# Performance work log

Hardware: AMD Instinct MI355X
Metric: run time of the kernel (lower is better)

Reference implementation:

```python
import jax, jax.numpy as jnp
import numpy as np

B, H, W, NF = 2, 80, 80, 128  # batch, height, width, n_filter
CIN = 2 * NF                  # input channels (final conv outputs 2*NF and adds to x)


def _conv(x, w):
    # 3x3, stride 1, SAME, no bias; NHWC / HWIO
    return jax.lax.conv_general_dilated(
        x, w, window_strides=(1, 1), padding='SAME',
        dimension_numbers=('NHWC', 'HWIO', 'NHWC'))


def setup_inputs() -> dict:
    key = jax.random.key(0)
    ks = jax.random.split(key, 5)
    def glorot(k, shape):
        fan_in = shape[0] * shape[1] * shape[2]
        fan_out = shape[0] * shape[1] * shape[3]
        lim = np.sqrt(6.0 / (fan_in + fan_out)).astype(np.float32)
        return jax.random.uniform(k, shape, jnp.float32, -lim, lim)
    return {
        'x': jax.random.normal(ks[0], (B, H, W, CIN), jnp.float32),
        'w_theta': glorot(ks[1], (3, 3, CIN, NF)),
        'w_phi':   glorot(ks[2], (3, 3, CIN, NF)),
        'w_g':     glorot(ks[3], (3, 3, CIN, NF)),
        'w_conv':  glorot(ks[4], (3, 3, NF, CIN)),
    }


def reference(x, w_theta, w_phi, w_g, w_conv):
    b, h, w, cin = x.shape
    c = w_theta.shape[-1]  # n_filter
    n = h * w
    theta = _conv(x, w_theta).reshape(b, n, c)        # (B, N, C)
    # NOTE: Keras Reshape((n_filter,-1)) is a row-major reshape, NOT a transpose
    phi = _conv(x, w_phi).reshape(b, c, n)            # (B, C, N)
    attn = jax.nn.softmax(jnp.einsum('bnc,bcm->bnm', theta, phi), axis=-1)  # (B, N, N)
    g = _conv(x, w_g).reshape(b, n, c)                # (B, N, C)
    out = jnp.einsum('bnm,bmc->bnc', attn, g).reshape(b, h, w, c)
    out = _conv(out, w_conv)                          # (B, H, W, 2C)
    return x + out
```

## Files before the change

### kernel.cpp

```cpp
#include <hip/hip_runtime.h>
#include <hip/hip_bf16.h>

#define HH_ 80
#define WW_ 80
#define CIN_ 256
#define NF_ 128
#define NPIX_ 6400
#define NTOK_ 12800
#define NELEM_ (NTOK_ * NF_)
#define NXEL_  (NTOK_ * CIN_)
#define KW_    2304
#define KWC_   1152
#define WEL_   294912

#define KVS_    8
#define KVB_    32
#define MCHUNK_ 800
#define NIT_    25

__device__ float g_theta[NELEM_];
__device__ float g_phi  [NELEM_];
__device__ float g_gv   [NELEM_];
__device__ unsigned short g_aob[NELEM_];
__device__ unsigned short g_th_hi[NELEM_], g_th_lo[NELEM_];
__device__ unsigned short g_phT_hi[NELEM_], g_phT_lo[NELEM_];
__device__ unsigned short g_gT[NELEM_];
__device__ float g_po [KVS_ * NELEM_];
__device__ float g_pml[KVS_ * NTOK_ * 2];
__device__ unsigned short g_xh[NXEL_], g_xl[NXEL_];
__device__ unsigned short g_wtTh[WEL_], g_wtTl[WEL_];
__device__ unsigned short g_wpTh[WEL_], g_wpTl[WEL_];
__device__ unsigned short g_wgT[WEL_];
__device__ unsigned short g_wcT[WEL_];

__device__ __forceinline__ float b2f(unsigned short u) {
    union { unsigned int i; float f; } v; v.i = ((unsigned int)u) << 16; return v.f;
}
__device__ __forceinline__ unsigned short f2b(float f) {
    union { float f; unsigned int i; } v; v.f = f;
    unsigned int i = v.i;
    i += 0x7fffu + ((i >> 16) & 1u);
    return (unsigned short)(i >> 16);
}

typedef __attribute__((ext_vector_type(8))) short bf16x8;
typedef __attribute__((ext_vector_type(4))) float f32x4;

__device__ __forceinline__ f32x4 mfma16(bf16x8 a, bf16x8 b, f32x4 c) {
    return __builtin_amdgcn_mfma_f32_16x16x32_bf16(a, b, c, 0, 0, 0);
}

__global__ __launch_bounds__(256) void prep_x(const float* __restrict__ x)
{
    const int i = (blockIdx.x * 256 + threadIdx.x) * 4;
    if (i >= NXEL_) return;
    const float4 v = *(const float4*)(x + i);
    ushort4 hi, lo;
    hi.x = f2b(v.x); lo.x = f2b(v.x - b2f(hi.x));
    hi.y = f2b(v.y); lo.y = f2b(v.y - b2f(hi.y));
    hi.z = f2b(v.z); lo.z = f2b(v.z - b2f(hi.z));
    hi.w = f2b(v.w); lo.w = f2b(v.w - b2f(hi.w));
    *(ushort4*)(g_xh + i) = hi;
    *(ushort4*)(g_xl + i) = lo;
}

__global__ __launch_bounds__(256) void prep_w(
    const float* __restrict__ wt, const float* __restrict__ wp,
    const float* __restrict__ wg, const float* __restrict__ wc)
{
    const int i = blockIdx.x * 256 + threadIdx.x;
    if (i >= WEL_) return;
    {
        const int t  = i / (256 * 128);
        const int r  = i % (256 * 128);
        const int ci = r >> 7;
        const int f  = r & 127;
        const size_t d = (size_t)(t * 8 + (ci >> 5)) * 4096
                       + (size_t)f * 32 + (ci & 31);
        const float tv = wt[i];
        const unsigned short th = f2b(tv);
        g_wtTh[d] = th; g_wtTl[d] = f2b(tv - b2f(th));
        const float pv = wp[i];
        const unsigned short ph = f2b(pv);
        g_wpTh[d] = ph; g_wpTl[d] = f2b(pv - b2f(ph));
        g_wgT[d] = f2b(wg[i]);
    }
    {
        const int t  = i / (128 * 256);
        const int r  = i % (128 * 256);
        const int ci = r >> 8;
        const int f  = r & 255;
        g_wcT[(size_t)f * KWC_ + t * 128 + ci] = f2b(wc[i]);
    }
}

__global__ __launch_bounds__(512) void conv3_mfma()
{
    __shared__ __align__(16) unsigned short w_lds[5][128][40];
    __shared__ __align__(16) unsigned short x_lds[64][2][40];

    const int tid  = threadIdx.x;
    const int wv   = tid >> 6;
    const int lane = tid & 63;
    const int quad = lane >> 4;
    const int ll   = lane & 15;
    const int wp   = wv >> 2;
    const int wf   = wv & 3;
    const int P0   = blockIdx.x * 64;
    const int fb   = wf * 32;

    const int sxp = tid >> 3;
    const int sxh = (tid >> 2) & 1;
    const int sxc = (tid & 3) * 8;
    const int swf = tid >> 2;
    const int swc = (tid & 3) * 8;

    const int sp  = P0 + sxp;
    const int spb = sp / NPIX_;
    const int spl = sp % NPIX_;
    const int sph = spl / WW_;
    const int spw = spl % WW_;

    const bf16x8 ZV = {0,0,0,0,0,0,0,0};
    bf16x8 rx, rw0, rw1, rw2, rw3, rw4;

#define C3_STAGE_LOAD(s)                                                      \
    {                                                                         \
        const int t_ = (s) >> 3, kc_ = (s) & 7;                               \
        const int hh_ = sph + t_ / 3 - 1, ww_ = spw + t_ % 3 - 1;             \
        if (hh_ >= 0 && hh_ < HH_ && ww_ >= 0 && ww_ < WW_) {                 \
            const size_t src_ = ((size_t)spb * NPIX_ + hh_ * WW_ + ww_) * CIN_\
                                + kc_ * 32 + sxc;                             \
            rx = sxh ? *(const bf16x8*)(g_xl + src_)                          \
                     : *(const bf16x8*)(g_xh + src_);                         \
        } else rx = ZV;                                                       \
        const size_t ws_ = (size_t)(s) * 4096 + (size_t)swf * 32 + swc;       \
        rw0 = *(const bf16x8*)(g_wtTh + ws_);                                 \
        rw1 = *(const bf16x8*)(g_wtTl + ws_);                                 \
        rw2 = *(const bf16x8*)(g_wpTh + ws_);                                 \
        rw3 = *(const bf16x8*)(g_wpTl + ws_);                                 \
        rw4 = *(const bf16x8*)(g_wgT  + ws_);                                 \
    }

#define C3_STAGE_WRITE()                                                      \
    {                                                                         \
        *(bf16x8*)(&x_lds[sxp][sxh][sxc]) = rx;                               \
        *(bf16x8*)(&w_lds[0][swf][swc]) = rw0;                                \
        *(bf16x8*)(&w_lds[1][swf][swc]) = rw1;                                \
        *(bf16x8*)(&w_lds[2][swf][swc]) = rw2;                                \
        *(bf16x8*)(&w_lds[3][swf][swc]) = rw3;                                \
        *(bf16x8*)(&w_lds[4][swf][swc]) = rw4;                                \
    }

    f32x4 aT[2][2], aP[2][2], aG[2][2];
    #pragma unroll
    for (int pt = 0; pt < 2; ++pt)
        #pragma unroll
        for (int ft = 0; ft < 2; ++ft) {
            aT[pt][ft] = (f32x4){0.f,0.f,0.f,0.f};
            aP[pt][ft] = (f32x4){0.f,0.f,0.f,0.f};
            aG[pt][ft] = (f32x4){0.f,0.f,0.f,0.f};
        }

    C3_STAGE_LOAD(0);
    C3_STAGE_WRITE();
    __syncthreads();

    for (int s = 0; s < 72; ++s) {
        const bool pf = (s + 1 < 72);
        if (pf) C3_STAGE_LOAD(s + 1);

        bf16x8 xa[2][2];
        #pragma unroll
        for (int pt = 0; pt < 2; ++pt) {
            const int px = wp * 32 + pt * 16 + ll;
            xa[pt][0] = *(const bf16x8*)(&x_lds[px][0][quad * 8]);
            xa[pt][1] = *(const bf16x8*)(&x_lds[px][1][quad * 8]);
        }
        #pragma unroll
        for (int ft = 0; ft < 2; ++ft) {
            const int f = fb + ft * 16 + ll;
            const bf16x8 tH = *(const bf16x8*)(&w_lds[0][f][quad * 8]);
            const bf16x8 tL = *(const bf16x8*)(&w_lds[1][f][quad * 8]);
            const bf16x8 pH = *(const bf16x8*)(&w_lds[2][f][quad * 8]);
            const bf16x8 pL = *(const bf16x8*)(&w_lds[3][f][quad * 8]);
            const bf16x8 gB = *(const bf16x8*)(&w_lds[4][f][quad * 8]);
            #pragma unroll
            for (int pt = 0; pt < 2; ++pt) {
                aT[pt][ft] = mfma16(xa[pt][0], tH, aT[pt][ft]);
                aT[pt][ft] = mfma16(xa[pt][0], tL, aT[pt][ft]);
                aT[pt][ft] = mfma16(xa[pt][1], tH, aT[pt][ft]);
                aP[pt][ft] = mfma16(xa[pt][0], pH, aP[pt][ft]);
                aP[pt][ft] = mfma16(xa[pt][0], pL, aP[pt][ft]);
                aP[pt][ft] = mfma16(xa[pt][1], pH, aP[pt][ft]);
                aG[pt][ft] = mfma16(xa[pt][0], gB, aG[pt][ft]);
            }
        }

        __syncthreads();
        if (pf) C3_STAGE_WRITE();
        __syncthreads();
    }

    #pragma unroll
    for (int pt = 0; pt < 2; ++pt)
        #pragma unroll
        for (int ft = 0; ft < 2; ++ft) {
            const int f = fb + ft * 16 + ll;
            #pragma unroll
            for (int r = 0; r < 4; ++r) {
                const size_t n = P0 + wp * 32 + pt * 16 + quad * 4 + r;
                g_theta[n * NF_ + f] = aT[pt][ft][r];
                g_phi  [n * NF_ + f] = aP[pt][ft][r];
                g_gv   [n * NF_ + f] = aG[pt][ft][r];
            }
        }
#undef C3_STAGE_LOAD
#undef C3_STAGE_WRITE
}

__global__ __launch_bounds__(256) void prep_pack()
{
    const int i = blockIdx.x * 256 + threadIdx.x;
    if (i >= NELEM_) return;
    const int n  = i >> 7;
    const int c  = i & 127;
    const int b  = n / NPIX_;
    const int nl = n % NPIX_;

    const float tv = g_theta[i];
    const unsigned short th = f2b(tv);
    g_th_hi[i] = th;
    g_th_lo[i] = f2b(tv - b2f(th));

    const float pv = g_phi[i];
    const int j  = nl * 128 + c;
    const int cp = j / NPIX_;
    const int mp = j % NPIX_;
    const unsigned short phh = f2b(pv);
    const size_t o = (size_t)b * (NPIX_ * NF_) + (size_t)mp * 128 + cp;
    g_phT_hi[o] = phh;
    g_phT_lo[o] = f2b(pv - b2f(phh));

    g_gT[(size_t)b * (NPIX_ * NF_) + (size_t)c * NPIX_ + nl] = f2b(g_gv[i]);
}

__global__ __launch_bounds__(256) void attn_mfma()
{
    __shared__ __align__(16) unsigned short kh_lds[KVB_][136];
    __shared__ __align__(16) unsigned short kl_lds[KVB_][136];
    __shared__ __align__(16) unsigned short v_lds[NF_][40];
    __shared__ __align__(16) short p_lds[4][16 * 40];

    const int tid  = threadIdx.x;
    const int w    = tid >> 6;
    const int lane = tid & 63;
    const int quad = lane >> 4;
    const int ll   = lane & 15;

    const int cid = blockIdx.x & 15;
    const int qw  = blockIdx.x >> 4;
    const int b   = cid >> 3;
    const int kvs = cid & 7;
    const int R0  = b * NPIX_ + qw * 64;
    const int m_start = kvs * MCHUNK_;

    const unsigned short* phH = g_phT_hi + (size_t)b * (NPIX_ * NF_);
    const unsigned short* phL = g_phT_lo + (size_t)b * (NPIX_ * NF_);
    const unsigned short* gT  = g_gT    + (size_t)b * (NPIX_ * NF_);

    bf16x8 aH[4], aL[4];
    #pragma unroll
    for (int kk = 0; kk < 4; ++kk) {
        const size_t off = (size_t)(R0 + w * 16 + ll) * 128 + kk * 32 + quad * 8;
        aH[kk] = *(const bf16x8*)(g_th_hi + off);
        aL[kk] = *(const bf16x8*)(g_th_lo + off);
    }

    f32x4 acc[8];
    #pragma unroll
    for (int t = 0; t < 8; ++t) acc[t] = (f32x4){0.f, 0.f, 0.f, 0.f};
    float mi = -1e30f, li = 0.f;

    const int kr0 = tid >> 4;
    const int kc0 = (tid & 15) * 8;
    const int vr0 = tid >> 2;
    const int vm0 = (tid & 3) * 8;

    bf16x8 skh0, skh1, skl0, skl1, sv0, sv1;

    {
        const int m0 = m_start;
        skh0 = *(const bf16x8*)(phH + (size_t)(m0 + kr0) * 128 + kc0);
        skh1 = *(const bf16x8*)(phH + (size_t)(m0 + kr0 + 16) * 128 + kc0);
        skl0 = *(const bf16x8*)(phL + (size_t)(m0 + kr0) * 128 + kc0);
        skl1 = *(const bf16x8*)(phL + (size_t)(m0 + kr0 + 16) * 128 + kc0);
        sv0  = *(const bf16x8*)(gT + (size_t)vr0 * NPIX_ + m0 + vm0);
        sv1  = *(const bf16x8*)(gT + (size_t)(vr0 + 64) * NPIX_ + m0 + vm0);
        *(bf16x8*)(&kh_lds[kr0][kc0])      = skh0;
        *(bf16x8*)(&kh_lds[kr0 + 16][kc0]) = skh1;
        *(bf16x8*)(&kl_lds[kr0][kc0])      = skl0;
        *(bf16x8*)(&kl_lds[kr0 + 16][kc0]) = skl1;
        *(bf16x8*)(&v_lds[vr0][vm0])       = sv0;
        *(bf16x8*)(&v_lds[vr0 + 64][vm0])  = sv1;
    }
    __syncthreads();

    short* pl = &p_lds[w][0];

    for (int it = 0; it < NIT_; ++it) {
        const bool pf = (it + 1 < NIT_);
        if (pf) {
            const int m0 = m_start + (it + 1) * KVB_;
            skh0 = *(const bf16x8*)(phH + (size_t)(m0 + kr0) * 128 + kc0);
            skh1 = *(const bf16x8*)(phH + (size_t)(m0 + kr0 + 16) * 128 + kc0);
            skl0 = *(const bf16x8*)(phL + (size_t)(m0 + kr0) * 128 + kc0);
            skl1 = *(const bf16x8*)(phL + (size_t)(m0 + kr0 + 16) * 128 + kc0);
            sv0  = *(const bf16x8*)(gT + (size_t)vr0 * NPIX_ + m0 + vm0);
            sv1  = *(const bf16x8*)(gT + (size_t)(vr0 + 64) * NPIX_ + m0 + vm0);
        }

        f32x4 s[2];
        #pragma unroll
        for (int mt = 0; mt < 2; ++mt) {
            f32x4 s0 = (f32x4){0.f,0.f,0.f,0.f};
            const int mrow = mt * 16 + ll;
            #pragma unroll
            for (int kk = 0; kk < 4; ++kk) {
                const bf16x8 bH = *(const bf16x8*)(&kh_lds[mrow][kk * 32 + quad * 8]);
                const bf16x8 bL = *(const bf16x8*)(&kl_lds[mrow][kk * 32 + quad * 8]);
                s0 = mfma16(bH, aH[kk], s0);
                s0 = mfma16(bL, aH[kk], s0);
                s0 = mfma16(bH, aL[kk], s0);
            }
            s[mt] = s0;
        }

        float cm = fmaxf(fmaxf(fmaxf(s[0][0], s[0][1]), fmaxf(s[0][2], s[0][3])),
                         fmaxf(fmaxf(s[1][0], s[1][1]), fmaxf(s[1][2], s[1][3])));
        cm = fmaxf(cm, __shfl_xor(cm, 16));
        cm = fmaxf(cm, __shfl_xor(cm, 32));
        const float nm = fmaxf(mi, cm);
        const float al = __expf(mi - nm);
        mi = nm;
        float ssum = 0.f;
        #pragma unroll
        for (int mt = 0; mt < 2; ++mt)
            #pragma unroll
            for (int r = 0; r < 4; ++r) {
                const float e = __expf(s[mt][r] - nm);
                s[mt][r] = e; ssum += e;
            }
        ssum += __shfl_xor(ssum, 16);
        ssum += __shfl_xor(ssum, 32);
        li = li * al + ssum;

        if (quad == 0)
            ((float*)(pl + (ll >> 2) * 40 + 32))[ll & 3] = al;

        #pragma unroll
        for (int mt = 0; mt < 2; ++mt)
            *(ushort4*)(pl + ll * 40 + mt * 16 + quad * 4) =
                make_ushort4(f2b(s[mt][0]), f2b(s[mt][1]),
                             f2b(s[mt][2]), f2b(s[mt][3]));

        {
            const float* alp = (const float*)(pl + quad * 40 + 32);
            #pragma unroll
            for (int r = 0; r < 4; ++r) {
                const float av = alp[r];
                #pragma unroll
                for (int t = 0; t < 8; ++t) acc[t][r] *= av;
            }
        }

        const bf16x8 pa = *(const bf16x8*)(pl + ll * 40 + quad * 8);

        #pragma unroll
        for (int ct = 0; ct < 8; ++ct) {
            const bf16x8 gb = *(const bf16x8*)(&v_lds[ct * 16 + ll][quad * 8]);
            acc[ct] = mfma16(pa, gb, acc[ct]);
        }

        __syncthreads();
        if (pf) {
            *(bf16x8*)(&kh_lds[kr0][kc0])      = skh0;
            *(bf16x8*)(&kh_lds[kr0 + 16][kc0]) = skh1;
            *(bf16x8*)(&kl_lds[kr0][kc0])      = skl0;
            *(bf16x8*)(&kl_lds[kr0 + 16][kc0]) = skl1;
            *(bf16x8*)(&v_lds[vr0][vm0])       = sv0;
            *(bf16x8*)(&v_lds[vr0 + 64][vm0])  = sv1;
        }
        __syncthreads();
    }

    const int row0 = R0 + w * 16;
    #pragma unroll
    for (int ct = 0; ct < 8; ++ct)
        #pragma unroll
        for (int r = 0; r < 4; ++r)
            g_po[((size_t)kvs * NTOK_ + row0 + quad * 4 + r) * NF_ + ct * 16 + ll]
                = acc[ct][r];
    if (quad == 0) {
        const size_t mlidx = ((size_t)kvs * NTOK_ + row0 + ll) * 2;
        g_pml[mlidx]     = mi;
        g_pml[mlidx + 1] = li;
    }
}

__global__ __launch_bounds__(256) void merge_attn()
{
    const int idx = blockIdx.x * 256 + threadIdx.x;
    const int row = idx >> 4;
    const int c0  = (idx & 15) * 8;

    float m[KVS_], l[KVS_];
    #pragma unroll
    for (int s = 0; s < KVS_; ++s) {
        const size_t mlidx = ((size_t)s * NTOK_ + row) * 2;
        m[s] = g_pml[mlidx];
        l[s] = g_pml[mlidx + 1];
    }
    float M = m[0];
    #pragma unroll
    for (int s = 1; s < KVS_; ++s) M = fmaxf(M, m[s]);
    float a[KVS_], L = 0.f;
    #pragma unroll
    for (int s = 0; s < KVS_; ++s) {
        a[s] = __expf(m[s] - M);
        L += a[s] * l[s];
    }
    const float inv = 1.f / L;

    float o[8];
    #pragma unroll
    for (int j = 0; j < 8; ++j) o[j] = 0.f;
    #pragma unroll
    for (int s = 0; s < KVS_; ++s) {
        const float* p = g_po + ((size_t)s * NTOK_ + row) * NF_ + c0;
        const float4 p0 = *(const float4*)(p);
        const float4 p1 = *(const float4*)(p + 4);
        o[0] += a[s] * p0.x; o[1] += a[s] * p0.y;
        o[2] += a[s] * p0.z; o[3] += a[s] * p0.w;
        o[4] += a[s] * p1.x; o[5] += a[s] * p1.y;
        o[6] += a[s] * p1.z; o[7] += a[s] * p1.w;
    }
    unsigned short tmp[8];
    #pragma unroll
    for (int j = 0; j < 8; ++j) tmp[j] = f2b(o[j] * inv);
    unsigned short* dst = g_aob + (size_t)row * NF_ + c0;
    *(ushort4*)(dst)     = make_ushort4(tmp[0], tmp[1], tmp[2], tmp[3]);
    *(ushort4*)(dst + 4) = make_ushort4(tmp[4], tmp[5], tmp[6], tmp[7]);
}

__global__ __launch_bounds__(256) void conv_out_mfma(
    const float* __restrict__ x, float* __restrict__ out)
{
    const int tid = threadIdx.x;
    const int w = tid >> 6, lane = tid & 63, quad = lane >> 4, ll = lane & 15;
    const int P0 = blockIdx.x * 32;
    const int fb = w * 64;

    int pb[2], ph[2], pw[2];
    #pragma unroll
    for (int pt = 0; pt < 2; ++pt) {
        const int p = P0 + pt * 16 + ll;
        pb[pt] = p / NPIX_;
        const int pl_ = p % NPIX_;
        ph[pt] = pl_ / WW_;
        pw[pt] = pl_ % WW_;
    }

    const bf16x8 ZV = {0,0,0,0,0,0,0,0};
    f32x4 acc[2][4];
    #pragma unroll
    for (int pt = 0; pt < 2; ++pt)
        #pragma unroll
        for (int ft = 0; ft < 4; ++ft) acc[pt][ft] = (f32x4){0.f,0.f,0.f,0.f};

    for (int t = 0; t < 9; ++t) {
        const int dh = t / 3 - 1, dw = t % 3 - 1;
        size_t abase[2]; bool av[2];
        #pragma unroll
        for (int pt = 0; pt < 2; ++pt) {
            const int hh = ph[pt] + dh, ww2 = pw[pt] + dw;
            av[pt] = (hh >= 0 && hh < HH_ && ww2 >= 0 && ww2 < WW_);
            abase[pt] = ((size_t)pb[pt] * NPIX_ + hh * WW_ + ww2) * NF_;
        }
        for (int kc = 0; kc < 4; ++kc) {
            const int ko = kc * 32 + quad * 8;
            bf16x8 a[2];
            #pragma unroll
            for (int pt = 0; pt < 2; ++pt)
                a[pt] = av[pt] ? *(const bf16x8*)(g_aob + abase[pt] + ko) : ZV;
            const int wk = t * 128 + ko;
            #pragma unroll
            for (int ft = 0; ft < 4; ++ft) {
                const bf16x8 bw = *(const bf16x8*)(
                    g_wcT + (size_t)(fb + ft * 16 + ll) * KWC_ + wk);
                #pragma unroll
                for (int pt = 0; pt < 2; ++pt)
                    acc[pt][ft] = mfma16(a[pt], bw, acc[pt][ft]);
            }
        }
    }

    #pragma unroll
    for (int pt = 0; pt < 2; ++pt)
        #pragma unroll
        for (int ft = 0; ft < 4; ++ft) {
            const int f = fb + ft * 16 + ll;
            #pragma unroll
            for (int r = 0; r < 4; ++r) {
                const size_t n = P0 + pt * 16 + quad * 4 + r;
                const size_t oi = n * CIN_ + f;
                out[oi] = x[oi] + acc[pt][ft][r];
            }
        }
}

extern "C" void kernel_launch(void* const* d_in, const int* in_sizes, int n_in,
                              void* d_out, int out_size, void* d_ws, size_t ws_size,
                              hipStream_t stream)
{
    const float* x  = (const float*)d_in[0];
    const float* wt = (const float*)d_in[1];
    const float* wp = (const float*)d_in[2];
    const float* wg = (const float*)d_in[3];
    const float* wc = (const float*)d_in[4];
    float* out = (float*)d_out;

    prep_x<<<NXEL_ / 4 / 256, 256, 0, stream>>>(x);
    prep_w<<<(WEL_ + 255) / 256, 256, 0, stream>>>(wt, wp, wg, wc);
    conv3_mfma<<<NTOK_ / 64, 512, 0, stream>>>();
    prep_pack<<<(NELEM_ + 255) / 256, 256, 0, stream>>>();
    attn_mfma<<<(NTOK_ / 64) * KVS_, 256, 0, stream>>>();
    merge_attn<<<NTOK_ * 16 / 256, 256, 0, stream>>>();
    conv_out_mfma<<<400, 256, 0, stream>>>(x, out);
}
```

Before: 406.5 us.

## Stage output conv through LDS with prefetch and add lazy softmax rescale

The output 3x3 conv now uses 512-thread blocks of 64 pixels. Weights and activation tiles are staged through shared memory with register prefetch of the next K-chunk, instead of every wave reading its weights straight from global memory, and the weight layout is rearranged to fit this. The attention inner loop skips the running-max update and accumulator rescale when no lane's new maximum exceeds the old one by more than 4, which saves exp and multiply work. It also converts P to bf16 with the packed v_cvt_pk_bf16_f32 instruction. The lazy rescale allows unnormalised exponents up to e^4, which may slightly change rounding, and the conv adds two block barriers per stage.

```diff
diff --git a/kernel.cpp b/kernel.cpp
--- a/kernel.cpp
+++ b/kernel.cpp
@@ -90,7 +90,9 @@
         const int r  = i % (128 * 256);
         const int ci = r >> 8;
         const int f  = r & 255;
-        g_wcT[(size_t)f * KWC_ + t * 128 + ci] = f2b(wc[i]);
+        const size_t d = (size_t)(t * 4 + (ci >> 5)) * 8192
+                       + (size_t)f * 32 + (ci & 31);
+        g_wcT[d] = f2b(wc[i]);
     }
 }
 
@@ -340,31 +342,38 @@
                          fmaxf(fmaxf(s[1][0], s[1][1]), fmaxf(s[1][2], s[1][3])));
         cm = fmaxf(cm, __shfl_xor(cm, 16));
         cm = fmaxf(cm, __shfl_xor(cm, 32));
-        const float nm = fmaxf(mi, cm);
-        const float al = __expf(mi - nm);
-        mi = nm;
+        const bool nog = __all(cm <= mi + 4.0f);
+        if (!nog) {
+            const float nm = fmaxf(mi, cm);
+            const float al = __expf(mi - nm);
+            mi = nm;
+            li *= al;
+            if (quad == 0)
+                ((float*)(pl + (ll >> 2) * 40 + 32))[ll & 3] = al;
+        }
         float ssum = 0.f;
         #pragma unroll
         for (int mt = 0; mt < 2; ++mt)
             #pragma unroll
             for (int r = 0; r < 4; ++r) {
-                const float e = __expf(s[mt][r] - nm);
+                const float e = __expf(s[mt][r] - mi);
                 s[mt][r] = e; ssum += e;
             }
         ssum += __shfl_xor(ssum, 16);
         ssum += __shfl_xor(ssum, 32);
-        li = li * al + ssum;
-
-        if (quad == 0)
-            ((float*)(pl + (ll >> 2) * 40 + 32))[ll & 3] = al;
-
-        #pragma unroll
-        for (int mt = 0; mt < 2; ++mt)
-            *(ushort4*)(pl + ll * 40 + mt * 16 + quad * 4) =
-                make_ushort4(f2b(s[mt][0]), f2b(s[mt][1]),
-                             f2b(s[mt][2]), f2b(s[mt][3]));
-
-        {
+        li += ssum;
+
+        #pragma unroll
+        for (int mt = 0; mt < 2; ++mt) {
+            unsigned int c0_, c1_;
+            asm("v_cvt_pk_bf16_f32 %0, %1, %2"
+                : "=v"(c0_) : "v"(s[mt][0]), "v"(s[mt][1]));
+            asm("v_cvt_pk_bf16_f32 %0, %1, %2"
+                : "=v"(c1_) : "v"(s[mt][2]), "v"(s[mt][3]));
+            *(uint2*)(pl + ll * 40 + mt * 16 + quad * 4) = make_uint2(c0_, c1_);
+        }
+
+        if (!nog) {
             const float* alp = (const float*)(pl + quad * 40 + 32);
             #pragma unroll
             for (int r = 0; r < 4; ++r) {
@@ -453,56 +462,88 @@
     *(ushort4*)(dst + 4) = make_ushort4(tmp[4], tmp[5], tmp[6], tmp[7]);
 }
 
-__global__ __launch_bounds__(256) void conv_out_mfma(
+__global__ __launch_bounds__(512) void conv_out_mfma(
     const float* __restrict__ x, float* __restrict__ out)
 {
-    const int tid = threadIdx.x;
-    const int w = tid >> 6, lane = tid & 63, quad = lane >> 4, ll = lane & 15;
-    const int P0 = blockIdx.x * 32;
-    const int fb = w * 64;
-
-    int pb[2], ph[2], pw[2];
-    #pragma unroll
-    for (int pt = 0; pt < 2; ++pt) {
-        const int p = P0 + pt * 16 + ll;
-        pb[pt] = p / NPIX_;
-        const int pl_ = p % NPIX_;
-        ph[pt] = pl_ / WW_;
-        pw[pt] = pl_ % WW_;
-    }
+    __shared__ __align__(16) unsigned short w_lds[256][40];
+    __shared__ __align__(16) unsigned short a_lds[64][40];
+
+    const int tid  = threadIdx.x;
+    const int wv   = tid >> 6;
+    const int lane = tid & 63;
+    const int quad = lane >> 4;
+    const int ll   = lane & 15;
+    const int wp   = wv >> 2;
+    const int wf   = wv & 3;
+    const int P0   = blockIdx.x * 64;
+    const int fb   = wf * 64;
+
+    const int swf = tid >> 1;
+    const int swc = (tid & 1) * 16;
+    const int sap = tid >> 2;
+    const int sac = (tid & 3) * 8;
+
+    const int sp  = P0 + sap;
+    const int spb = sp / NPIX_;
+    const int spl = sp % NPIX_;
+    const int sph = spl / WW_;
+    const int spw = spl % WW_;
 
     const bf16x8 ZV = {0,0,0,0,0,0,0,0};
+    bf16x8 ra, rwA, rwB;
+
+#define CO_STAGE_LOAD(s)                                                      \
+    {                                                                         \
+        const int t_ = (s) >> 2, kc_ = (s) & 3;                               \
+        if (tid < 256) {                                                      \
+            const int hh_ = sph + t_ / 3 - 1, ww_ = spw + t_ % 3 - 1;         \
+            if (hh_ >= 0 && hh_ < HH_ && ww_ >= 0 && ww_ < WW_) {             \
+                const size_t src_ = ((size_t)spb * NPIX_ + hh_ * WW_ + ww_)   \
+                                    * NF_ + kc_ * 32 + sac;                   \
+                ra = *(const bf16x8*)(g_aob + src_);                          \
+            } else ra = ZV;                                                   \
+        }                                                                     \
+        const size_t ws_ = (size_t)(s) * 8192 + (size_t)swf * 32 + swc;       \
+        rwA = *(const bf16x8*)(g_wcT + ws_);                                  \
+        rwB = *(const bf16x8*)(g_wcT + ws_ + 8);                              \
+    }
+
+#define CO_STAGE_WRITE()                                                      \
+    {                                                                         \
+        if (tid < 256) *(bf16x8*)(&a_lds[sap][sac]) = ra;                     \
+        *(bf16x8*)(&w_lds[swf][swc])     = rwA;                               \
+        *(bf16x8*)(&w_lds[swf][swc + 8]) = rwB;                               \
+    }
+
     f32x4 acc[2][4];
     #pragma unroll
     for (int pt = 0; pt < 2; ++pt)
         #pragma unroll
         for (int ft = 0; ft < 4; ++ft) acc[pt][ft] = (f32x4){0.f,0.f,0.f,0.f};
 
-    for (int t = 0; t < 9; ++t) {
-        const int dh = t / 3 - 1, dw = t % 3 - 1;
-        size_t abase[2]; bool av[2];
-        #pragma unroll
-        for (int pt = 0; pt < 2; ++pt) {
-            const int hh = ph[pt] + dh, ww2 = pw[pt] + dw;
-            av[pt] = (hh >= 0 && hh < HH_ && ww2 >= 0 && ww2 < WW_);
-            abase[pt] = ((size_t)pb[pt] * NPIX_ + hh * WW_ + ww2) * NF_;
-        }
-        for (int kc = 0; kc < 4; ++kc) {
-            const int ko = kc * 32 + quad * 8;
-            bf16x8 a[2];
+    CO_STAGE_LOAD(0);
+    CO_STAGE_WRITE();
+    __syncthreads();
+
+    for (int s = 0; s < 36; ++s) {
+        const bool pf = (s + 1 < 36);
+        if (pf) CO_STAGE_LOAD(s + 1);
+
+        bf16x8 a[2];
+        #pragma unroll
+        for (int pt = 0; pt < 2; ++pt)
+            a[pt] = *(const bf16x8*)(&a_lds[wp * 32 + pt * 16 + ll][quad * 8]);
+        #pragma unroll
+        for (int ft = 0; ft < 4; ++ft) {
+            const bf16x8 bw = *(const bf16x8*)(&w_lds[fb + ft * 16 + ll][quad * 8]);
             #pragma unroll
             for (int pt = 0; pt < 2; ++pt)
-                a[pt] = av[pt] ? *(const bf16x8*)(g_aob + abase[pt] + ko) : ZV;
-            const int wk = t * 128 + ko;
-            #pragma unroll
-            for (int ft = 0; ft < 4; ++ft) {
-                const bf16x8 bw = *(const bf16x8*)(
-                    g_wcT + (size_t)(fb + ft * 16 + ll) * KWC_ + wk);
-                #pragma unroll
-                for (int pt = 0; pt < 2; ++pt)
-                    acc[pt][ft] = mfma16(a[pt], bw, acc[pt][ft]);
-            }
-        }
+                acc[pt][ft] = mfma16(a[pt], bw, acc[pt][ft]);
+        }
+
+        __syncthreads();
+        if (pf) CO_STAGE_WRITE();
+        __syncthreads();
     }
 
     #pragma unroll
@@ -512,11 +553,13 @@
             const int f = fb + ft * 16 + ll;
             #pragma unroll
             for (int r = 0; r < 4; ++r) {
-                const size_t n = P0 + pt * 16 + quad * 4 + r;
+                const size_t n = P0 + wp * 32 + pt * 16 + quad * 4 + r;
                 const size_t oi = n * CIN_ + f;
                 out[oi] = x[oi] + acc[pt][ft][r];
             }
         }
+#undef CO_STAGE_LOAD
+#undef CO_STAGE_WRITE
 }
 
 extern "C" void kernel_launch(void* const* d_in, const int* in_sizes, int n_in,
@@ -536,5 +579,5 @@
     prep_pack<<<(NELEM_ + 255) / 256, 256, 0, stream>>>();
     attn_mfma<<<(NTOK_ / 64) * KVS_, 256, 0, stream>>>();
     merge_attn<<<NTOK_ * 16 / 256, 256, 0, stream>>>();
-    conv_out_mfma<<<400, 256, 0, stream>>>(x, out);
-}
+    conv_out_mfma<<<NTOK_ / 64, 512, 0, stream>>>(x, out);
+}
```

Result: faster. 376.0 us (-7.5%).
